# Optimization experiments

Hardware: AMD Instinct MI355X
Metric: run time of the kernel (lower is better)

The kernel has to match this reference:

```python
import jax, jax.numpy as jnp
import numpy as np

D_MODEL = 1024
NUM_HEADS = 16
HEAD_DIM = D_MODEL // NUM_HEADS
THETA = 10000.0
MAX_SEQ_LEN = 2048
BATCH = 4
SEQ = 2048


def _rope_tables():
    # theta_vec = 1 / theta**(arange(0, d_k, 2)/d_k), pos outer product
    inv_freq = 1.0 / (THETA ** (jnp.arange(0, HEAD_DIM, 2, dtype=jnp.float32) / HEAD_DIM))
    pos = jnp.arange(MAX_SEQ_LEN, dtype=jnp.float32)
    freqs = jnp.outer(pos, inv_freq)  # [max_seq, head_dim//2]
    return jnp.cos(freqs), jnp.sin(freqs)


def apply_rope(x, cos, sin):
    # x: [..., S, d]; cos/sin: [S, d//2]; interleaved pairwise rotation
    x1 = x[..., 0::2]
    x2 = x[..., 1::2]
    o1 = x1 * cos - x2 * sin
    o2 = x2 * cos + x1 * sin
    return jnp.stack([o1, o2], axis=-1).reshape(x.shape)


def setup_inputs() -> dict:
    key = jax.random.key(0)
    kx, kq, kk, kv, ko = jax.random.split(key, 5)
    std = (1.0 / D_MODEL) ** 0.5
    x = jax.random.normal(kx, (BATCH, SEQ, D_MODEL), dtype=jnp.float32)
    w_q = jax.random.normal(kq, (D_MODEL, D_MODEL), dtype=jnp.float32) * std
    w_k = jax.random.normal(kk, (D_MODEL, D_MODEL), dtype=jnp.float32) * std
    w_v = jax.random.normal(kv, (D_MODEL, D_MODEL), dtype=jnp.float32) * std
    w_o = jax.random.normal(ko, (D_MODEL, D_MODEL), dtype=jnp.float32) * std
    cos, sin = _rope_tables()
    return {"x": x, "w_q": w_q, "w_k": w_k, "w_v": w_v, "w_o": w_o,
            "cos": cos, "sin": sin}


def reference(x, w_q, w_k, w_v, w_o, cos, sin):
    b, s, d = x.shape
    h, dk = NUM_HEADS, HEAD_DIM

    def proj(w):
        # einsum '... s d, hd d -> ... s hd' == x @ w.T, then split heads
        y = jnp.einsum('bsd,ed->bse', x, w)
        return y.reshape(b, s, h, dk).transpose(0, 2, 1, 3)  # [b,h,s,dk]

    q = apply_rope(proj(w_q), cos[:s], sin[:s])
    k = apply_rope(proj(w_k), cos[:s], sin[:s])
    v = proj(w_v)

    scores = jnp.einsum('bhnd,bhmd->bhnm', q, k) / (dk ** 0.5)
    causal = jnp.tril(jnp.ones((s, s), dtype=bool))
    scores = jnp.where(causal, scores, -jnp.inf)
    attn = jax.nn.softmax(scores, axis=-1)
    out = jnp.einsum('bhnm,bhmd->bhnd', attn, v)  # [b,h,s,dk]
    out = out.transpose(0, 2, 1, 3).reshape(b, s, d)
    # einsum '... s hd, d hd -> ... s d' == out @ w_o.T
    return jnp.einsum('bse,de->bsd', out, w_o)
```

## Files before the change

kernel.cpp:

```cpp
#include <hip/hip_runtime.h>
#include <hip/hip_bf16.h>


typedef __bf16 bf16;
typedef __bf16 bf16x8 __attribute__((ext_vector_type(8)));
typedef __bf16 bf16x4 __attribute__((ext_vector_type(4)));
typedef float f32x4 __attribute__((ext_vector_type(4)));

#define LOG2E 1.4426950408889634f
#define QSCALE (0.125f * LOG2E * 8388608.0f)
#define SEXP_SEED ((126.94269504f - 16.0f * LOG2E) * 8388608.0f)

__device__ __forceinline__ void async16(const void* g, void* l) {
  __builtin_amdgcn_global_load_lds(
      (const __attribute__((address_space(1))) void*)g,
      (__attribute__((address_space(3))) void*)l, 16, 0, 0);
}

#define MFMA16(a, b, c) __builtin_amdgcn_mfma_f32_16x16x32_bf16(a, b, c, 0, 0, 0)

__global__ void cast_all_kernel(const float* __restrict__ x,
                                const float* __restrict__ wq,
                                const float* __restrict__ wk,
                                const float* __restrict__ wv,
                                const float* __restrict__ wo,
                                const float* __restrict__ cosT,
                                const float* __restrict__ sinT,
                                bf16* __restrict__ xb, bf16* __restrict__ wb,
                                float2* __restrict__ csT) {
  int i = blockIdx.x * blockDim.x + threadIdx.x;
  if (i >= 3145728) {
    int j = i - 3145728;
    float2 cs;
    cs.x = cosT[j];
    cs.y = sinT[j];
    csT[j] = cs;
    return;
  }
  const float* src;
  bf16* dst;
  long o;
  if (i < 2097152) {
    src = x; dst = xb; o = i;
  } else {
    long j = i - 2097152;
    int w = (int)(j >> 18);
    o = j & 262143;
    src = (w == 0) ? wq : (w == 1) ? wk : (w == 2) ? wv : wo;
    dst = wb + (long)w * 1048576;
  }
  float4 v = reinterpret_cast<const float4*>(src)[o];
  bf16x4 out;
  out.x = (bf16)v.x; out.y = (bf16)v.y; out.z = (bf16)v.z; out.w = (bf16)v.w;
  *reinterpret_cast<bf16x4*>(dst + o * 4) = out;
}

template <int EPI, int TM, int TN>
__device__ __forceinline__ void gemm_dev(const bf16* __restrict__ A,
                                         const bf16* __restrict__ B,
                                         void* __restrict__ C, int N, int K,
                                         int ldk, int bm, int bn, bf16* As,
                                         bf16* Bs,
                                         const float2* __restrict__ csT) {
  constexpr int WM = TM / 64;
  constexpr int WN = 4 / WM;
  constexpr int CW = TN / WN;
  constexpr int NT = CW / 16;
  constexpr int ROUNDS = (TM + TN) / 32;
  const int tid = threadIdx.x;
  const int wid = tid >> 6, lane = tid & 63;
  const int quad = lane >> 4, l15 = lane & 15;
  const int waveM = wid / WN, waveN = wid % WN;

  f32x4 acc[4][NT] = {};
  const bf16* Ag = A + (long)bm * TM * ldk;
  const bf16* Bg = B + (long)bn * TN * ldk;

  for (int k0 = 0; k0 < K; k0 += 64) {
#pragma unroll
    for (int ri = 0; ri < ROUNDS; ++ri) {
      int ci = ri * 256 + tid;
      int gb = ri * 256 + (wid << 6);
      bool isA = gb < TM * 8;
      int cl = isA ? ci : ci - TM * 8;
      int r = cl >> 3;
      int col = ((cl & 7) ^ (r & 7)) << 3;
      const bf16* src = (isA ? Ag : Bg) + (long)r * ldk + k0 + col;
      char* dst = isA ? ((char*)As + (long)ci * 16)
                      : ((char*)Bs + (long)(ci - TM * 8) * 16);
      async16(src, dst);
    }
    __syncthreads();
#pragma unroll
    for (int kk = 0; kk < 2; ++kk) {
      bf16x8 af[4], bfr[NT];
#pragma unroll
      for (int t = 0; t < 4; ++t) {
        int rowA = waveM * 64 + t * 16 + l15;
        af[t] = *(const bf16x8*)(As + rowA * 64 +
                                 ((((kk << 2) + quad) ^ (rowA & 7)) << 3));
      }
#pragma unroll
      for (int t = 0; t < NT; ++t) {
        int rowB = waveN * CW + t * 16 + l15;
        bfr[t] = *(const bf16x8*)(Bs + rowB * 64 +
                                  ((((kk << 2) + quad) ^ (rowB & 7)) << 3));
      }
#pragma unroll
      for (int mt = 0; mt < 4; ++mt)
#pragma unroll
        for (int nt = 0; nt < NT; ++nt)
          acc[mt][nt] = MFMA16(af[mt], bfr[nt], acc[mt][nt]);
    }
    if (k0 + 64 < K) __syncthreads();
  }

  const float qsc = (EPI == 0 && bn < 8) ? QSCALE : 1.0f;
#pragma unroll
  for (int mt = 0; mt < 4; ++mt)
#pragma unroll
    for (int nt = 0; nt < NT; ++nt)
#pragma unroll
      for (int r = 0; r < 4; ++r) {
        int row = bm * TM + waveM * 64 + mt * 16 + quad * 4 + r;
        int col = bn * TN + waveN * CW + nt * 16 + l15;
        float v = acc[mt][nt][r];
        if (EPI == 0) {
          float pr = __shfl_xor(v, 1);
          int d = col & 63;
          float2 cs = csT[(row & 2047) * 32 + (d >> 1)];
          float o =
              (col & 1) ? (v * cs.x + pr * cs.y) : (v * cs.x - pr * cs.y);
          o *= qsc;
          long off = (long)(col >> 10) * 8388608 +
                     (long)(((row >> 11) << 4) + ((col >> 6) & 15)) * 131072 +
                     (long)(row & 2047) * 64 + d;
          ((bf16*)C)[off] = (bf16)o;
        } else if (EPI == 1) {
          long off = (long)(col >> 11) * 2097152 + (long)row * 2048 +
                     (col & 2047);
          ((bf16*)C)[off] = (bf16)v;
        } else if (EPI == 2) {
          ((float*)C)[(long)row * N + col] = v;
        } else {
          atomicAdd(&((float*)C)[(long)row * N + col], v);
        }
      }
}

__global__ __launch_bounds__(256) void gemm_qkv(const bf16* __restrict__ xb,
                                                const bf16* __restrict__ wqk,
                                                const bf16* __restrict__ wv,
                                                bf16* __restrict__ QK,
                                                bf16* __restrict__ VT,
                                                const float2* __restrict__ csT) {
  __shared__ __align__(16) bf16 As[128 * 64];
  __shared__ __align__(16) bf16 Bs[128 * 64];
  int p = blockIdx.x;
  if (p >= 1024) {
    int pv = p - 1024;
    int lv = (pv & 7) * 64 + (pv >> 3);
    gemm_dev<1, 128, 128>(wv, xb, VT, 8192, 1024, 1024, lv & 7, lv >> 3, As,
                          Bs, nullptr);
  } else {
    int l = (p & 7) * 128 + (p >> 3);
    gemm_dev<0, 128, 128>(xb, wqk, QK, 2048, 1024, 1024, l >> 4, l & 15, As,
                          Bs, csT);
  }
}

__global__ __launch_bounds__(256) void gemm_out(const bf16* __restrict__ A,
                                                const bf16* __restrict__ B,
                                                float* __restrict__ C) {
  __shared__ __align__(16) bf16 As[128 * 64];
  __shared__ __align__(16) bf16 Bs[128 * 64];
  int p = blockIdx.x;
  int kh = p >> 9;
  int t = p & 511;
  int l = (t & 7) * 64 + (t >> 3);
  gemm_dev<3, 128, 128>(A + kh * 512, B + kh * 512, C, 1024, 512, 1024,
                        l >> 3, l & 7, As, Bs, nullptr);
}

__device__ __forceinline__ void pack_row(const f32x4& s, bf16* Pw, int l15,
                                         int mt, int quad) {
  int i0 = (int)s[0], i1 = (int)s[1], i2 = (int)s[2], i3 = (int)s[3];
  uint2 pk;
  pk.x = __builtin_amdgcn_perm((unsigned)i1, (unsigned)i0, 0x07060302u);
  pk.y = __builtin_amdgcn_perm((unsigned)i3, (unsigned)i2, 0x07060302u);
  *(uint2*)(Pw + l15 * 88 + mt * 16 + quad * 4) = pk;
}

__device__ __forceinline__ void attn_step(const bf16* Ks, const bf16* Vs,
                                          bf16* Pw, const bf16x8* qf,
                                          const bf16x8 ones, f32x4* accO,
                                          f32x4& accL, int quad, int l15,
                                          int qloc, bool diag) {
  const int sw = l15 & 7;
  const f32x4 seedv = {SEXP_SEED, SEXP_SEED, SEXP_SEED, SEXP_SEED};
#pragma unroll
  for (int mt = 0; mt < 4; ++mt) {
    f32x4 s = seedv;
#pragma unroll
    for (int kk = 0; kk < 2; ++kk) {
      bf16x8 kf = *(const bf16x8*)(Ks + (mt * 16 + l15) * 64 +
                                   ((((kk << 2) + quad) ^ sw) << 3));
      s = MFMA16(kf, qf[kk], s);
    }
    if (diag) {
#pragma unroll
      for (int r = 0; r < 4; ++r)
        if ((mt * 16 + quad * 4 + r) > qloc) s[r] = 0.0f;
    }
    pack_row(s, Pw, l15, mt, quad);
  }
  asm volatile("s_waitcnt lgkmcnt(0)" ::: "memory");
  bf16x8 pfr[2];
#pragma unroll
  for (int kk = 0; kk < 2; ++kk)
    pfr[kk] = *(const bf16x8*)(Pw + l15 * 88 + kk * 32 + quad * 8);
#pragma unroll
  for (int nt = 0; nt < 4; ++nt)
#pragma unroll
    for (int kk = 0; kk < 2; ++kk) {
      bf16x8 vf = *(const bf16x8*)(Vs + (nt * 16 + l15) * 64 +
                                   ((((kk << 2) + quad) ^ sw) << 3));
      accO[nt] = MFMA16(pfr[kk], vf, accO[nt]);
    }
#pragma unroll
  for (int kk = 0; kk < 2; ++kk)
    accL = MFMA16(pfr[kk], ones, accL);
}

__device__ __forceinline__ void attn_step2(
    const bf16* Ks, const bf16* Vs, bf16* Pw1, bf16* Pw0, const bf16x8* qf1,
    const bf16x8* qf0, const bf16x8 ones, f32x4* acc1, f32x4* acc0,
    f32x4& accL1, f32x4& accL0, int quad, int l15, int qloc, bool diag0) {
  const int sw = l15 & 7;
  const f32x4 seedv = {SEXP_SEED, SEXP_SEED, SEXP_SEED, SEXP_SEED};
#pragma unroll
  for (int mt = 0; mt < 4; ++mt) {
    f32x4 s1 = seedv, s0 = seedv;
#pragma unroll
    for (int kk = 0; kk < 2; ++kk) {
      bf16x8 kf = *(const bf16x8*)(Ks + (mt * 16 + l15) * 64 +
                                   ((((kk << 2) + quad) ^ sw) << 3));
      s1 = MFMA16(kf, qf1[kk], s1);
      s0 = MFMA16(kf, qf0[kk], s0);
    }
    if (diag0) {
#pragma unroll
      for (int r = 0; r < 4; ++r)
        if ((mt * 16 + quad * 4 + r) > qloc) s0[r] = 0.0f;
    }
    pack_row(s1, Pw1, l15, mt, quad);
    pack_row(s0, Pw0, l15, mt, quad);
  }
  asm volatile("s_waitcnt lgkmcnt(0)" ::: "memory");
  bf16x8 pf1[2], pf0[2];
#pragma unroll
  for (int kk = 0; kk < 2; ++kk) {
    pf1[kk] = *(const bf16x8*)(Pw1 + l15 * 88 + kk * 32 + quad * 8);
    pf0[kk] = *(const bf16x8*)(Pw0 + l15 * 88 + kk * 32 + quad * 8);
  }
#pragma unroll
  for (int nt = 0; nt < 4; ++nt)
#pragma unroll
    for (int kk = 0; kk < 2; ++kk) {
      bf16x8 vf = *(const bf16x8*)(Vs + (nt * 16 + l15) * 64 +
                                   ((((kk << 2) + quad) ^ sw) << 3));
      acc1[nt] = MFMA16(pf1[kk], vf, acc1[nt]);
      acc0[nt] = MFMA16(pf0[kk], vf, acc0[nt]);
    }
#pragma unroll
  for (int kk = 0; kk < 2; ++kk) {
    accL1 = MFMA16(pf1[kk], ones, accL1);
    accL0 = MFMA16(pf0[kk], ones, accL0);
  }
}

__global__ __launch_bounds__(256, 4) void attn_kernel(
    const bf16* __restrict__ Q, const bf16* __restrict__ Kg,
    const bf16* __restrict__ VT, bf16* __restrict__ Out) {
  __shared__ __align__(16) bf16 Ks[64 * 64];
  __shared__ __align__(16) bf16 Vs[64 * 64];
  __shared__ __align__(16) bf16 Ps[4][2][16 * 88];
  const int tid = threadIdx.x, wid = tid >> 6, lane = tid & 63;
  const int quad = lane >> 4, l15 = lane & 15;
  const int id = blockIdx.x;
  const int p = (id >> 3) & 15;
  const int bh = (id & 7) * 8 + (id >> 7);
  const int q0t = p, q1t = 31 - p;
  const bf16* Qb = Q + (long)bh * 131072;
  const bf16* Kb = Kg + (long)bh * 131072;
  const bf16* Vb = VT + (long)bh * 131072;
  bf16* Pw1 = &Ps[wid][0][0];
  bf16* Pw0 = &Ps[wid][1][0];
  const int qloc = wid * 16 + l15;

  bf16x8 ones;
#pragma unroll
  for (int j = 0; j < 8; ++j) ones[j] = (bf16)1.0f;

  bf16x8 qf0[2], qf1[2];
#pragma unroll
  for (int kk = 0; kk < 2; ++kk) {
    qf0[kk] = *(const bf16x8*)(Qb + (long)(q0t * 64 + qloc) * 64 + kk * 32 +
                               quad * 8);
    qf1[kk] = *(const bf16x8*)(Qb + (long)(q1t * 64 + qloc) * 64 + kk * 32 +
                               quad * 8);
  }
  f32x4 acc0[4] = {}, acc1[4] = {};
  f32x4 accL0 = {}, accL1 = {};

  for (int kt = 0; kt <= q1t; ++kt) {
#pragma unroll
    for (int it = 0; it < 2; ++it) {
      int chunk = it * 256 + tid;
      int r = chunk >> 3;
      int c = (((chunk & 7) ^ (r & 7)) << 3);
      int ldsbase = (it * 256 + wid * 64) * 16;
      async16(Kb + (long)(kt * 64 + r) * 64 + c, (char*)Ks + ldsbase);
      async16(Vb + (long)r * 2048 + kt * 64 + c, (char*)Vs + ldsbase);
    }
    __syncthreads();
    if (kt <= q0t)
      attn_step2(Ks, Vs, Pw1, Pw0, qf1, qf0, ones, acc1, acc0, accL1, accL0,
                 quad, l15, qloc, kt == q0t);
    else
      attn_step(Ks, Vs, Pw1, qf1, ones, acc1, accL1, quad, l15, qloc,
                kt == q1t);
    __syncthreads();
  }

  const int b = bh >> 4, h = bh & 15;
#pragma unroll
  for (int r = 0; r < 4; ++r) {
    float lr0 = 1.0f / accL0[r];
    float lr1 = 1.0f / accL1[r];
#pragma unroll
    for (int nt = 0; nt < 4; ++nt) {
      int d = h * 64 + nt * 16 + l15;
      int qg0 = q0t * 64 + wid * 16 + quad * 4 + r;
      int qg1 = q1t * 64 + wid * 16 + quad * 4 + r;
      Out[(long)(b * 2048 + qg0) * 1024 + d] = (bf16)(acc0[nt][r] * lr0);
      Out[(long)(b * 2048 + qg1) * 1024 + d] = (bf16)(acc1[nt][r] * lr1);
    }
  }
}

extern "C" void kernel_launch(void* const* d_in, const int* in_sizes, int n_in,
                              void* d_out, int out_size, void* d_ws,
                              size_t ws_size, hipStream_t stream) {
  const float* x = (const float*)d_in[0];
  const float* w_q = (const float*)d_in[1];
  const float* w_k = (const float*)d_in[2];
  const float* w_v = (const float*)d_in[3];
  const float* w_o = (const float*)d_in[4];
  const float* cosT = (const float*)d_in[5];
  const float* sinT = (const float*)d_in[6];

  char* ws = (char*)d_ws;
  bf16* xb = (bf16*)(ws + 0);
  bf16* wqb = (bf16*)(ws + 16777216);
  bf16* wvb = (bf16*)(ws + 20971520);
  bf16* wob = (bf16*)(ws + 23068672);
  bf16* Qb = (bf16*)(ws + 25165824);
  bf16* Kb = (bf16*)(ws + 41943040);
  bf16* VTb = (bf16*)(ws + 58720256);
  float2* csT = (float2*)(ws + 75497472);
  bf16* attnb = xb;

  cast_all_kernel<<<12544, 256, 0, stream>>>(x, w_q, w_k, w_v, w_o, cosT,
                                             sinT, xb, wqb, csT);

  hipMemsetAsync(d_out, 0, (size_t)out_size, stream);

  gemm_qkv<<<1536, 256, 0, stream>>>(xb, wqb, wvb, Qb, VTb, csT);

  attn_kernel<<<1024, 256, 0, stream>>>(Qb, Kb, VTb, attnb);

  gemm_out<<<1024, 256, 0, stream>>>(attnb, wob, (float*)d_out);
}
```

Before: 286.3 us.

## Replace split-K atomic output GEMM with direct 128x64 tiles; batch QK MFMAs

The output projection stops splitting K in two halves with atomicAdd into a zeroed buffer. It now runs full-K 128x64 tiles that store fp32 results directly, which removes the memset and the atomic traffic. The attention inner step also issues all four QK^T MFMA chains before masking and packing, to expose more independent MFMAs. The risk is that the new GEMM tile uses smaller N tiles with a longer K loop per block, which lowers reuse per block.

```diff
diff --git a/kernel.cpp b/kernel.cpp
--- a/kernel.cpp
+++ b/kernel.cpp
@@ -59,8 +59,7 @@
 __device__ __forceinline__ void gemm_dev(const bf16* __restrict__ A,
                                          const bf16* __restrict__ B,
                                          void* __restrict__ C, int N, int K,
-                                         int ldk, int bm, int bn, bf16* As,
-                                         bf16* Bs,
+                                         int bm, int bn, bf16* As, bf16* Bs,
                                          const float2* __restrict__ csT) {
   constexpr int WM = TM / 64;
   constexpr int WN = 4 / WM;
@@ -73,8 +72,8 @@
   const int waveM = wid / WN, waveN = wid % WN;
 
   f32x4 acc[4][NT] = {};
-  const bf16* Ag = A + (long)bm * TM * ldk;
-  const bf16* Bg = B + (long)bn * TN * ldk;
+  const bf16* Ag = A + (long)bm * TM * K;
+  const bf16* Bg = B + (long)bn * TN * K;
 
   for (int k0 = 0; k0 < K; k0 += 64) {
 #pragma unroll
@@ -85,7 +84,7 @@
       int cl = isA ? ci : ci - TM * 8;
       int r = cl >> 3;
       int col = ((cl & 7) ^ (r & 7)) << 3;
-      const bf16* src = (isA ? Ag : Bg) + (long)r * ldk + k0 + col;
+      const bf16* src = (isA ? Ag : Bg) + (long)r * K + k0 + col;
       char* dst = isA ? ((char*)As + (long)ci * 16)
                       : ((char*)Bs + (long)(ci - TM * 8) * 16);
       async16(src, dst);
@@ -140,10 +139,8 @@
           long off = (long)(col >> 11) * 2097152 + (long)row * 2048 +
                      (col & 2047);
           ((bf16*)C)[off] = (bf16)v;
-        } else if (EPI == 2) {
+        } else {
           ((float*)C)[(long)row * N + col] = v;
-        } else {
-          atomicAdd(&((float*)C)[(long)row * N + col], v);
         }
       }
 }
@@ -160,12 +157,12 @@
   if (p >= 1024) {
     int pv = p - 1024;
     int lv = (pv & 7) * 64 + (pv >> 3);
-    gemm_dev<1, 128, 128>(wv, xb, VT, 8192, 1024, 1024, lv & 7, lv >> 3, As,
-                          Bs, nullptr);
+    gemm_dev<1, 128, 128>(wv, xb, VT, 8192, 1024, lv & 7, lv >> 3, As, Bs,
+                          nullptr);
   } else {
     int l = (p & 7) * 128 + (p >> 3);
-    gemm_dev<0, 128, 128>(xb, wqk, QK, 2048, 1024, 1024, l >> 4, l & 15, As,
-                          Bs, csT);
+    gemm_dev<0, 128, 128>(xb, wqk, QK, 2048, 1024, l >> 4, l & 15, As, Bs,
+                          csT);
   }
 }
 
@@ -173,13 +170,10 @@
                                                 const bf16* __restrict__ B,
                                                 float* __restrict__ C) {
   __shared__ __align__(16) bf16 As[128 * 64];
-  __shared__ __align__(16) bf16 Bs[128 * 64];
+  __shared__ __align__(16) bf16 Bs[64 * 64];
   int p = blockIdx.x;
-  int kh = p >> 9;
-  int t = p & 511;
-  int l = (t & 7) * 64 + (t >> 3);
-  gemm_dev<3, 128, 128>(A + kh * 512, B + kh * 512, C, 1024, 512, 1024,
-                        l >> 3, l & 7, As, Bs, nullptr);
+  int l = (p & 7) * 128 + (p >> 3);
+  gemm_dev<2, 128, 64>(A, B, C, 1024, 1024, l >> 4, l & 15, As, Bs, nullptr);
 }
 
 __device__ __forceinline__ void pack_row(const f32x4& s, bf16* Pw, int l15,
@@ -198,22 +192,24 @@
                                           int qloc, bool diag) {
   const int sw = l15 & 7;
   const f32x4 seedv = {SEXP_SEED, SEXP_SEED, SEXP_SEED, SEXP_SEED};
-#pragma unroll
-  for (int mt = 0; mt < 4; ++mt) {
-    f32x4 s = seedv;
+  f32x4 sacc[4] = {seedv, seedv, seedv, seedv};
+#pragma unroll
+  for (int mt = 0; mt < 4; ++mt)
 #pragma unroll
     for (int kk = 0; kk < 2; ++kk) {
       bf16x8 kf = *(const bf16x8*)(Ks + (mt * 16 + l15) * 64 +
                                    ((((kk << 2) + quad) ^ sw) << 3));
-      s = MFMA16(kf, qf[kk], s);
-    }
-    if (diag) {
+      sacc[mt] = MFMA16(kf, qf[kk], sacc[mt]);
+    }
+  if (diag) {
+#pragma unroll
+    for (int mt = 0; mt < 4; ++mt)
 #pragma unroll
       for (int r = 0; r < 4; ++r)
-        if ((mt * 16 + quad * 4 + r) > qloc) s[r] = 0.0f;
-    }
-    pack_row(s, Pw, l15, mt, quad);
-  }
+        if ((mt * 16 + quad * 4 + r) > qloc) sacc[mt][r] = 0.0f;
+  }
+#pragma unroll
+  for (int mt = 0; mt < 4; ++mt) pack_row(sacc[mt], Pw, l15, mt, quad);
   asm volatile("s_waitcnt lgkmcnt(0)" ::: "memory");
   bf16x8 pfr[2];
 #pragma unroll
@@ -374,8 +370,6 @@
   cast_all_kernel<<<12544, 256, 0, stream>>>(x, w_q, w_k, w_v, w_o, cosT,
                                              sinT, xb, wqb, csT);
 
-  hipMemsetAsync(d_out, 0, (size_t)out_size, stream);
-
   gemm_qkv<<<1536, 256, 0, stream>>>(xb, wqb, wvb, Qb, VTb, csT);
 
   attn_kernel<<<1024, 256, 0, stream>>>(Qb, Kb, VTb, attnb);
```

After: 247.9 us. 1.15x faster.
